# Kernel tuning notes

Measured on AMD Instinct MI355X. Metric: run time of the kernel, lower is better.

The kernel has to match this reference:

```python
import jax, jax.numpy as jnp
import numpy as np

# Module config (init_kwargs), window_type='1d' (forward default)
GROUPS = 4
WIN = (1, 9)      # search_window_1d (ps_y, ps_x)
DIL = (1, 1)      # search_dilate_1d
S = WIN[0] * WIN[1]  # search_pixels = 9

B, C, H, W = 2, 256, 80, 160


def setup_inputs() -> dict:
    key = jax.random.key(0)
    k1, k2, k3, k4 = jax.random.split(key, 4)
    return {
        "left_feature": jax.random.normal(k1, (B, C, H, W), jnp.float32),
        "right_feature": jax.random.normal(k2, (B, C, H, W), jnp.float32),
        "flow": jax.random.normal(k3, (B, 2, H, W), jnp.float32) * 2.0,
        "extra_offset": jax.random.normal(k4, (B, 2 * S, H, W), jnp.float32),
    }


def _window_offsets():
    # torch.meshgrid(arange(-rx,rx+1,dx), arange(-ry,ry+1,dy), indexing='xy')
    ry, rx = (WIN[0] // 2) * DIL[0], (WIN[1] // 2) * DIL[1]
    xg, yg = np.meshgrid(np.arange(-rx, rx + 1, DIL[1]),
                         np.arange(-ry, ry + 1, DIL[0]), indexing="xy")
    off = np.stack([xg, yg], 0).reshape(2, -1).T  # (S, 2) as (x, y)
    return jnp.asarray(off, jnp.float32)


def _bilinear_sample(img, coords):
    """F.grid_sample(mode='bilinear', padding_mode='zeros', align_corners=True)
    with absolute pixel coords (torchvision raft's grid_sample normalizes by
    2*x/(W-1)-1, which is exactly identity sampling at absolute coords).
    img: (B,C,H,W); coords: (B,S,H,W,2) absolute (x,y). Returns (B,C,S,H,W)."""
    Bv, Cv, Hv, Wv = img.shape
    x, y = coords[..., 0], coords[..., 1]
    x0f = jnp.floor(x); y0f = jnp.floor(y)
    wx = (x - x0f)[:, None]  # (B,1,S,H,W)
    wy = (y - y0f)[:, None]
    x0 = x0f.astype(jnp.int32); y0 = y0f.astype(jnp.int32)
    imgf = img.reshape(Bv, Cv, Hv * Wv)

    def gather(yi, xi):
        valid = (xi >= 0) & (xi < Wv) & (yi >= 0) & (yi < Hv)
        idx = jnp.clip(yi, 0, Hv - 1) * Wv + jnp.clip(xi, 0, Wv - 1)
        v = jax.vmap(lambda im, ix: im[:, ix])(imgf, idx)  # (B,C,S,H,W)
        return v * valid[:, None].astype(img.dtype)

    v00 = gather(y0, x0)
    v01 = gather(y0, x0 + 1)
    v10 = gather(y0 + 1, x0)
    v11 = gather(y0 + 1, x0 + 1)
    return (v00 * (1 - wx) * (1 - wy) + v01 * wx * (1 - wy)
            + v10 * (1 - wx) * wy + v11 * wx * wy)


def reference(left_feature, right_feature, flow, extra_offset):
    Bv, Cv, Hv, Wv = left_feature.shape
    gC = Cv // GROUPS
    # make_coords_grid: channel order (x, y), absolute pixel coords
    yy, xx = jnp.meshgrid(jnp.arange(Hv, dtype=jnp.float32),
                          jnp.arange(Wv, dtype=jnp.float32), indexing="ij")
    base = jnp.stack([xx, yy], -1)[None, None] \
        + jnp.transpose(flow, (0, 2, 3, 1))[:, None]            # (B,1,H,W,2)
    extra = jnp.transpose(extra_offset.reshape(Bv, S, 2, Hv, Wv),
                          (0, 1, 3, 4, 2))                        # (B,S,H,W,2)
    coords = base + _window_offsets()[None, :, None, None, :] + extra
    # All groups share identical window/dilation, so sample all channels once.
    sampled = _bilinear_sample(right_feature, coords)  # (B,C,S,H,W)
    leftg = left_feature.reshape(Bv, GROUPS, gC, Hv, Wv)
    sampg = sampled.reshape(Bv, GROUPS, gC, S, Hv, Wv)
    # mean over group channels of left * sampled
    corr = jnp.einsum("bgchw,bgcshw->bgshw", leftg, sampg) / gC
    return corr.reshape(Bv, GROUPS * S, Hv, Wv)
```

## Files before the change

### kernel.cpp

```cpp
#include <hip/hip_runtime.h>

#define Bc   2
#define Cc   256
#define Hc   80
#define Wc   160
#define Gc   4
#define Sc   9
#define GCc  64
#define HWc  (Hc * Wc)
#define H2c  (Hc / 2)
#define WTc  (Wc / 32)
#define NW   4
#define CPW  16

#define PROWS   20
#define TSTRIDE 68
#define TDW     (PROWS * TSTRIDE)

typedef float f4 __attribute__((ext_vector_type(4)));
typedef _Float16 h2 __attribute__((ext_vector_type(2)));
typedef unsigned u4 __attribute__((ext_vector_type(4)));

static __device__ __forceinline__ unsigned pk(float a, float b) {
    return __builtin_bit_cast(unsigned, __builtin_amdgcn_cvt_pkrtz(a, b));
}
static __device__ __forceinline__ float dot2(unsigned w, unsigned v, float c) {
#if __has_builtin(__builtin_amdgcn_fdot2)
    return __builtin_amdgcn_fdot2(__builtin_bit_cast(h2, w),
                                  __builtin_bit_cast(h2, v), c, false);
#else
    h2 hw = __builtin_bit_cast(h2, w), hv = __builtin_bit_cast(h2, v);
    return c + (float)hw[0] * (float)hv[0] + (float)hw[1] * (float)hv[1];
#endif
}

#define CFENCE() asm volatile("" ::: "memory")

#define ITER2(cI, RV, LV, BUF)                                              \
  do {                                                                      \
    asm volatile("s_waitcnt lgkmcnt(0)" ::: "memory");                      \
    _Pragma("unroll")                                                       \
    for (int j = 0; j < 5; ++j) {                                           \
      unsigned* q = twBase + (BUF) * TDW + (5 * ls + j) * TSTRIDE + seg * 4;\
      u4 val = { pk(RV[j][0], RV[j + 1][0]), pk(RV[j][1], RV[j + 1][1]),    \
                 pk(RV[j][2], RV[j + 1][2]), pk(RV[j][3], RV[j + 1][3]) };  \
      *(u4*)q = val;      \
    }                                                                       \
    CFENCE();                                                               \
    if ((cI) + 2 < CPW) {                                                   \
      const float* Rn = Rb + (size_t)((cI) + 2) * HWc;                      \
      _Pragma("unroll")                                                     \
      for (int k = 0; k < 6; ++k) RV[k] = *(const f4*)(Rn + rowEl[k]);      \
    }                                                                       \
    {                                                                       \
      const unsigned* twr = twBase + (BUF) * TDW;                           \
      _Pragma("unroll")                                                     \
      for (int s = 0; s < Sc; ++s) {                                        \
        const unsigned d0 = twr[idx[s]];                                    \
        const unsigned d1 = twr[idx[s] + 1];                                \
        float sd = dot2(wA[s], d0, 0.0f);                                   \
        sd = dot2(wB[s], d1, sd);                                           \
        acc[s] = fmaf(LV, sd, acc[s]);                                      \
      }                                                                     \
    }                                                                       \
    if ((cI) + 2 < CPW) LV = Lb[(size_t)((cI) + 2) * HWc];                  \
  } while (0)

__global__ __launch_bounds__(256, 3)
void aoc_corr_kernel(const float* __restrict__ left,
                     const float* __restrict__ right,
                     const float* __restrict__ flow,
                     const float* __restrict__ extra,
                     float* __restrict__ out)
{
    __shared__ unsigned tile[NW][2][TDW];

    const int p = blockIdx.x;
    int bid = 200 * (p & 7) + (p >> 3);

    int wt = bid % WTc; bid /= WTc;
    int h2i = bid % H2c; bid /= H2c;
    int g  = bid % Gc;  bid /= Gc;
    int b  = bid;

    const int tid  = threadIdx.x;
    const int wid  = tid >> 6;
    const int lane = tid & 63;
    const int r    = lane >> 5;
    const int col  = lane & 31;
    const int h    = h2i * 2 + r;
    const int w    = wt * 32 + col;
    const int pix  = h * Wc + w;

    const float* flowb = flow + (size_t)b * 2 * HWc;
    const float bx = (float)w + flowb[pix];
    const float by = (float)h + flowb[HWc + pix];

    int   xb9[Sc], y09[Sc], y19[Sc];
    float w00[Sc], w01[Sc], w10[Sc], w11[Sc];
    int minX = 1 << 30, maxX = -(1 << 30), minY = 1 << 30, maxY = -(1 << 30);

    const float* exb = extra + (size_t)b * (2 * Sc) * HWc + pix;
#pragma unroll
    for (int s = 0; s < Sc; ++s) {
        const float ex = exb[(size_t)(2 * s) * HWc];
        const float ey = exb[(size_t)(2 * s + 1) * HWc];
        const float x = bx + (float)(s - 4) + ex;
        const float y = by + ey;

        const float x0f = floorf(x);
        const float y0f = floorf(y);
        const float fx = x - x0f;
        const float fy = y - y0f;
        const int x0 = (int)x0f;
        const int y0 = (int)y0f;
        const int y1 = y0 + 1;

        const int xb = min(max(x0, 0), Wc - 2);
        const float cA = (x0 == xb) ? (1.0f - fx) : ((x0 == -1)     ? fx          : 0.0f);
        const float cB = (x0 == xb) ? fx          : ((x0 == Wc - 1) ? (1.0f - fx) : 0.0f);
        const float r0 = (y0 >= 0 && y0 < Hc) ? (1.0f - fy) : 0.0f;
        const float r1 = (y1 >= 0 && y1 < Hc) ? fy          : 0.0f;
        const int yc0 = min(max(y0, 0), Hc - 1);
        const int yc1 = min(max(y1, 0), Hc - 1);

        w00[s] = cA * r0;  w01[s] = cB * r0;
        w10[s] = cA * r1;  w11[s] = cB * r1;
        xb9[s] = xb;  y09[s] = yc0;  y19[s] = yc1;

        minX = min(minX, xb);
        maxX = max(maxX, xb);
        minY = min(minY, min(yc0, yc1));
        maxY = max(maxY, max(yc0, yc1));
    }

#pragma unroll
    for (int k = 1; k < 64; k <<= 1) {
        minX = min(minX, __shfl_xor(minX, k));
        maxX = max(maxX, __shfl_xor(maxX, k));
        minY = min(minY, __shfl_xor(minY, k));
        maxY = max(maxY, __shfl_xor(maxY, k));
    }
    const int minX2 = min(minX, Wc - 64) & ~3;
    const bool valid = (maxY - minY + 1 <= PROWS) && (maxX - minX2 <= 62);

    const float* Rb = right + ((size_t)b * Cc + (size_t)(g * GCc + wid * CPW)) * HWc;
    const float* Lb = left  + ((size_t)b * Cc + (size_t)(g * GCc + wid * CPW)) * HWc + pix;

    float acc[Sc];
#pragma unroll
    for (int s = 0; s < Sc; ++s) acc[s] = 0.0f;

    if (valid) {
        unsigned wA[Sc], wB[Sc];
        int idx[Sc];
#pragma unroll
        for (int s = 0; s < Sc; ++s) {
            const int t  = y09[s] - minY;
            const int sB = y19[s] - y09[s];
            const float A0 = w00[s] + (sB ? 0.0f : w10[s]);
            const float A1 = sB ? w10[s] : 0.0f;
            const float B0 = w01[s] + (sB ? 0.0f : w11[s]);
            const float B1 = sB ? w11[s] : 0.0f;
            wA[s] = pk(A0, A1);
            wB[s] = pk(B0, B1);
            idx[s] = t * TSTRIDE + (xb9[s] - minX2);
        }

        const int ls  = lane >> 4;
        const int seg = lane & 15;
        int rowEl[6];
#pragma unroll
        for (int k = 0; k < 6; ++k)
            rowEl[k] = min(minY + 5 * ls + k, Hc - 1) * Wc + minX2 + seg * 4;

        unsigned* twBase = &tile[wid][0][0];

        f4 rvE[6], rvO[6];
#pragma unroll
        for (int k = 0; k < 6; ++k) rvE[k] = *(const f4*)(Rb + rowEl[k]);
#pragma unroll
        for (int k = 0; k < 6; ++k) rvO[k] = *(const f4*)(Rb + HWc + rowEl[k]);
        float lvE = Lb[0];
        float lvO = Lb[HWc];

#pragma unroll 1
        for (int cc = 0; cc < CPW; cc += 2) {
            ITER2(cc,     rvE, lvE, 0);
            ITER2(cc + 1, rvO, lvO, 1);
        }
    } else {
        int offA[Sc], offB[Sc];
#pragma unroll
        for (int s = 0; s < Sc; ++s) {
            offA[s] = y09[s] * Wc + xb9[s];
            offB[s] = y19[s] * Wc + xb9[s];
        }
        for (int c = 0; c < CPW; ++c) {
            const float lv = Lb[(size_t)c * HWc];
            const float* Rc = Rb + (size_t)c * HWc;
#pragma unroll
            for (int s = 0; s < Sc; ++s) {
                const float vA0 = Rc[offA[s]];
                const float vA1 = Rc[offA[s] + 1];
                const float vB0 = Rc[offB[s]];
                const float vB1 = Rc[offB[s] + 1];
                acc[s] += lv * (w00[s] * vA0 + w01[s] * vA1 +
                                w10[s] * vB0 + w11[s] * vB1);
            }
        }
    }

    float* red = (float*)&tile[0][0][0];
    __syncthreads();
    if (wid != 0) {
#pragma unroll
        for (int s = 0; s < Sc; ++s)
            red[((wid - 1) * Sc + s) * 64 + lane] = acc[s];
    }
    __syncthreads();
    if (wid == 0) {
        const float inv = 1.0f / (float)GCc;
        float* ob = out + ((size_t)b * Gc + g) * Sc * HWc + pix;
#pragma unroll
        for (int s = 0; s < Sc; ++s) {
            float v = acc[s];
#pragma unroll
            for (int ww = 1; ww < NW; ++ww)
                v += red[((ww - 1) * Sc + s) * 64 + lane];
            ob[(size_t)s * HWc] = v * inv;
        }
    }
}

extern "C" void kernel_launch(void* const* d_in, const int* in_sizes, int n_in,
                              void* d_out, int out_size, void* d_ws, size_t ws_size,
                              hipStream_t stream) {
    const float* left  = (const float*)d_in[0];
    const float* right = (const float*)d_in[1];
    const float* flow  = (const float*)d_in[2];
    const float* extra = (const float*)d_in[3];
    float* out = (float*)d_out;

    const int nblocks = Bc * Gc * H2c * WTc;
    aoc_corr_kernel<<<nblocks, NW * 64, 0, stream>>>(left, right, flow, extra, out);
}
```

Baseline: 49.71 us.

## Deepen channel prefetch to three register buffers and fully unroll loop

Moves the global-load prefetch of right-feature rows from two to three channels ahead, using three register buffer sets, and fully unrolls the 16-channel loop. It drops the explicit lgkmcnt(0) wait before the LDS writes and leaves that ordering to the compiler, and lowers the launch-bounds occupancy hint from 3 to 2 blocks to give room for the extra registers. The aim is to hide more global memory latency, at the cost of lower occupancy and relying on compiler-inserted waits for correctness of the double-buffered LDS tile reuse.

```diff
diff --git a/kernel.cpp b/kernel.cpp
--- a/kernel.cpp
+++ b/kernel.cpp
@@ -36,9 +36,9 @@
 
 #define CFENCE() asm volatile("" ::: "memory")
 
-#define ITER2(cI, RV, LV, BUF)                                              \
+#define ITER3(cI, RV, LV, BUF)                                              \
   do {                                                                      \
-    asm volatile("s_waitcnt lgkmcnt(0)" ::: "memory");                      \
+    CFENCE();                                                               \
     _Pragma("unroll")                                                       \
     for (int j = 0; j < 5; ++j) {                                           \
       unsigned* q = twBase + (BUF) * TDW + (5 * ls + j) * TSTRIDE + seg * 4;\
@@ -47,8 +47,8 @@
       *(u4*)q = val;      \
     }                                                                       \
     CFENCE();                                                               \
-    if ((cI) + 2 < CPW) {                                                   \
-      const float* Rn = Rb + (size_t)((cI) + 2) * HWc;                      \
+    if ((cI) + 3 < CPW) {                                                   \
+      const float* Rn = Rb + (size_t)((cI) + 3) * HWc;                      \
       _Pragma("unroll")                                                     \
       for (int k = 0; k < 6; ++k) RV[k] = *(const f4*)(Rn + rowEl[k]);      \
     }                                                                       \
@@ -63,10 +63,10 @@
         acc[s] = fmaf(LV, sd, acc[s]);                                      \
       }                                                                     \
     }                                                                       \
-    if ((cI) + 2 < CPW) LV = Lb[(size_t)((cI) + 2) * HWc];                  \
+    if ((cI) + 3 < CPW) LV = Lb[(size_t)((cI) + 3) * HWc];                  \
   } while (0)
 
-__global__ __launch_bounds__(256, 3)
+__global__ __launch_bounds__(256, 2)
 void aoc_corr_kernel(const float* __restrict__ left,
                      const float* __restrict__ right,
                      const float* __restrict__ flow,
@@ -176,19 +176,33 @@
 
         unsigned* twBase = &tile[wid][0][0];
 
-        f4 rvE[6], rvO[6];
-#pragma unroll
-        for (int k = 0; k < 6; ++k) rvE[k] = *(const f4*)(Rb + rowEl[k]);
-#pragma unroll
-        for (int k = 0; k < 6; ++k) rvO[k] = *(const f4*)(Rb + HWc + rowEl[k]);
-        float lvE = Lb[0];
-        float lvO = Lb[HWc];
-
-#pragma unroll 1
-        for (int cc = 0; cc < CPW; cc += 2) {
-            ITER2(cc,     rvE, lvE, 0);
-            ITER2(cc + 1, rvO, lvO, 1);
-        }
+        f4 rvA[6], rvB[6], rvC[6];
+#pragma unroll
+        for (int k = 0; k < 6; ++k) rvA[k] = *(const f4*)(Rb + rowEl[k]);
+#pragma unroll
+        for (int k = 0; k < 6; ++k) rvB[k] = *(const f4*)(Rb + HWc + rowEl[k]);
+#pragma unroll
+        for (int k = 0; k < 6; ++k) rvC[k] = *(const f4*)(Rb + 2 * HWc + rowEl[k]);
+        float lvA = Lb[0];
+        float lvB = Lb[HWc];
+        float lvC = Lb[2 * (size_t)HWc];
+
+        ITER3( 0, rvA, lvA, 0);
+        ITER3( 1, rvB, lvB, 1);
+        ITER3( 2, rvC, lvC, 0);
+        ITER3( 3, rvA, lvA, 1);
+        ITER3( 4, rvB, lvB, 0);
+        ITER3( 5, rvC, lvC, 1);
+        ITER3( 6, rvA, lvA, 0);
+        ITER3( 7, rvB, lvB, 1);
+        ITER3( 8, rvC, lvC, 0);
+        ITER3( 9, rvA, lvA, 1);
+        ITER3(10, rvB, lvB, 0);
+        ITER3(11, rvC, lvC, 1);
+        ITER3(12, rvA, lvA, 0);
+        ITER3(13, rvB, lvB, 1);
+        ITER3(14, rvC, lvC, 0);
+        ITER3(15, rvA, lvA, 1);
     } else {
         int offA[Sc], offB[Sc];
 #pragma unroll
```

After: 47.92 us. 3.6% less time.
